# Kernel optimization log

Measured on AMD Instinct MI355X. Metric: run time of the kernel, lower is better.

## Reference

```python
import jax, jax.numpy as jnp
import numpy as np
import math

VOCAB, D, L, B, S = 32000, 1024, 6, 4, 1024
FF = 4 * D


def sinusoidal_pe(max_len, d_model):
    pos = np.arange(max_len)[:, None].astype(np.float32)
    div = np.exp(np.arange(0, d_model, 2).astype(np.float32) * (-math.log(10000.0) / d_model))
    pe = np.zeros((max_len, d_model), dtype=np.float32)
    pe[:, 0::2] = np.sin(pos * div)
    pe[:, 1::2] = np.cos(pos * div)
    return jnp.asarray(pe)


def layernorm(x, g, b, eps=1e-5):
    mu = jnp.mean(x, axis=-1, keepdims=True)
    var = jnp.mean(jnp.square(x - mu), axis=-1, keepdims=True)
    return (x - mu) * jax.lax.rsqrt(var + eps) * g + b


def setup_inputs() -> dict:
    key = jax.random.key(0)
    ks = jax.random.split(key, 16)
    s = 0.02
    inp = {
        "input_ids": jax.random.randint(ks[0], (B, S), 0, VOCAB, dtype=jnp.int32),
        "attention_mask": jnp.ones((B, S), dtype=jnp.int32),
        "emb": jax.random.normal(ks[1], (VOCAB, D), jnp.float32) * s,
        "Wq": jax.random.normal(ks[2], (L, D, D), jnp.float32) * s,
        "Wk": jax.random.normal(ks[3], (L, D, D), jnp.float32) * s,
        "Wv": jax.random.normal(ks[4], (L, D, D), jnp.float32) * s,
        "bq": jnp.zeros((L, D), jnp.float32),
        "bk": jnp.zeros((L, D), jnp.float32),
        "bv": jnp.zeros((L, D), jnp.float32),
        "g1": jnp.ones((L, D), jnp.float32),
        "beta1": jnp.zeros((L, D), jnp.float32),
        "Wf1": jax.random.normal(ks[5], (L, D, FF), jnp.float32) * s,
        "bf1": jnp.zeros((L, FF), jnp.float32),
        "Wf2": jax.random.normal(ks[6], (L, FF, D), jnp.float32) * s,
        "bf2": jnp.zeros((L, D), jnp.float32),
        "g2": jnp.ones((L, D), jnp.float32),
        "beta2": jnp.zeros((L, D), jnp.float32),
    }
    return inp


def reference(input_ids, attention_mask, emb, Wq, Wk, Wv, bq, bk, bv,
              g1, beta1, Wf1, bf1, Wf2, bf2, g2, beta2):
    pe = sinusoidal_pe(1024, D)
    x = emb[input_ids] + pe[: input_ids.shape[1]]           # [B,S,D]
    mask = (attention_mask[:, None, :] != 0)                # [B,1,S]
    scale = 1.0 / math.sqrt(D)
    for l in range(L):
        Q = jnp.einsum('bsd,de->bse', x, Wq[l]) + bq[l]
        K = jnp.einsum('bsd,de->bse', x, Wk[l]) + bk[l]
        V = jnp.einsum('bsd,de->bse', x, Wv[l]) + bv[l]
        scores = jnp.einsum('bqd,bkd->bqk', Q, K) * scale   # [B,S,S]
        scores = jnp.where(mask, scores, -1e9)
        attn = jax.nn.softmax(scores, axis=-1)
        a = jnp.einsum('bqk,bkd->bqd', attn, V)
        x = layernorm(x + a, g1[l], beta1[l])
        h = jax.nn.relu(jnp.einsum('bsd,df->bsf', x, Wf1[l]) + bf1[l])
        f = jnp.einsum('bsf,fd->bsd', h, Wf2[l]) + bf2[l]
        x = layernorm(x + f, g2[l], beta2[l])
    return x
```

## Files before the change

kernel.cpp:

```cpp
#include <hip/hip_runtime.h>

typedef __bf16 bf16_t;
typedef __bf16 bf16x8 __attribute__((ext_vector_type(8)));
typedef float f32x4 __attribute__((ext_vector_type(4)));
typedef unsigned short u16;

#define DEV static __device__ __forceinline__

DEV float bf2f(u16 u) { __bf16 h = __builtin_bit_cast(__bf16, u); return (float)h; }
DEV u16 f2bf(float f) { __bf16 h = (__bf16)f; return __builtin_bit_cast(u16, h); }

DEV void gll16(bf16_t* lds, const bf16_t* g) {
    __builtin_amdgcn_global_load_lds(
        (const __attribute__((address_space(1))) void*)g,
        (__attribute__((address_space(3))) void*)lds, 16, 0, 0);
}

#define WAITV(N) asm volatile("s_waitcnt vmcnt(" #N ")" ::: "memory")

template <int EPI>
__global__ __launch_bounds__(512, 1)
void gemm8p(const bf16_t* __restrict__ A, int lda,
            const bf16_t* __restrict__ Bt, int ldb,
            bf16_t* __restrict__ C, int ldc,
            const float* __restrict__ bias, int K,
            long kadv, long cadv)
{
    __shared__ bf16_t Asm[2 * 2 * 8192];
    __shared__ bf16_t Bsm[2 * 2 * 8192];
    const int tid = threadIdx.x, w = tid >> 6, l = tid & 63;
    const int z = blockIdx.z;
    A  += (size_t)z * kadv;
    Bt += (size_t)z * kadv;
    C  += (size_t)z * cadv;

    const int gx = gridDim.x;
    int lin = blockIdx.y * gx + blockIdx.x;
    const int nlin = gx * gridDim.y;
    lin = (lin & 7) * (nlin >> 3) + (lin >> 3);
    const size_t row0 = (size_t)(lin / gx) * 256;
    const size_t col0 = (size_t)(lin % gx) * 256;

    const int wr = w >> 2, wc = w & 3;
    const int bh = wc >> 1;
    const int browoff = (wc & 1) * 64;
    const int fr = l & 15, q = l >> 4, sw = l & 7;

    const int srow = w * 8 + (l >> 3);
    const int sslot8 = ((l & 7) ^ ((l >> 3) & 7)) * 8;
    const bf16_t* AgH0 = A  + (row0 + srow) * (size_t)lda + sslot8;
    const bf16_t* BgH0 = Bt + (col0 + srow) * (size_t)ldb + sslot8;
    const size_t a128 = (size_t)128 * lda, b128 = (size_t)128 * ldb;
    const size_t a64  = (size_t)64 * lda,  b64  = (size_t)64 * ldb;
    const int wlds = w * 512;

#define STAGE_PAIR(buf, tt, p)                                                 \
    do {                                                                       \
        const int koff = (tt) * 64;                                            \
        if ((p) == 0) {                                                        \
            gll16(Asm + ((buf)*2+0)*8192 + wlds,        AgH0 + koff);          \
            gll16(Asm + ((buf)*2+0)*8192 + 4096 + wlds, AgH0 + koff + a64);    \
        } else if ((p) == 1) {                                                 \
            gll16(Asm + ((buf)*2+1)*8192 + wlds,        AgH0 + a128 + koff);   \
            gll16(Asm + ((buf)*2+1)*8192 + 4096 + wlds, AgH0 + a128 + koff + a64); \
        } else if ((p) == 2) {                                                 \
            gll16(Bsm + ((buf)*2+0)*8192 + wlds,        BgH0 + koff);          \
            gll16(Bsm + ((buf)*2+0)*8192 + 4096 + wlds, BgH0 + koff + b64);    \
        } else {                                                               \
            gll16(Bsm + ((buf)*2+1)*8192 + wlds,        BgH0 + b128 + koff);   \
            gll16(Bsm + ((buf)*2+1)*8192 + 4096 + wlds, BgH0 + b128 + koff + b64); \
        }                                                                      \
    } while (0)

    f32x4 acc[8][4] = {};
    const int NT = K >> 6;

    STAGE_PAIR(0, 0, 0); STAGE_PAIR(0, 0, 1); STAGE_PAIR(0, 0, 2); STAGE_PAIR(0, 0, 3);
    if (NT > 1) { STAGE_PAIR(1, 1, 0); WAITV(2); } else { WAITV(0); }
    __builtin_amdgcn_sched_barrier(0);
    __builtin_amdgcn_s_barrier();

    bf16x8 aR[4][2], bR[4][2];
    for (int t = 0; t < NT; ++t) {
        const int cur = t & 1, nxt = cur ^ 1;
        const bool hasN1 = (t + 1 < NT), hasN2 = (t + 2 < NT);
        const bf16_t* Ab = Asm + (cur * 2 + wr) * 8192;
        const bf16_t* Bb = Bsm + (cur * 2 + bh) * 8192;

#pragma unroll
        for (int mi = 0; mi < 4; mi++)
#pragma unroll
            for (int kk = 0; kk < 2; kk++)
                aR[mi][kk] = *(const bf16x8*)&Ab[(mi * 16 + fr) * 64 + ((kk * 4 + q) ^ sw) * 8];
#pragma unroll
        for (int ni = 0; ni < 2; ni++)
#pragma unroll
            for (int kk = 0; kk < 2; kk++)
                bR[ni][kk] = *(const bf16x8*)&Bb[(browoff + ni * 16 + fr) * 64 + ((kk * 4 + q) ^ sw) * 8];
        if (hasN1) STAGE_PAIR(nxt, t + 1, 1);
        __builtin_amdgcn_s_barrier();
        __builtin_amdgcn_s_setprio(1);
#pragma unroll
        for (int mi = 0; mi < 4; mi++)
#pragma unroll
            for (int ni = 0; ni < 2; ni++)
#pragma unroll
                for (int kk = 0; kk < 2; kk++)
                    acc[mi][ni] = __builtin_amdgcn_mfma_f32_16x16x32_bf16(aR[mi][kk], bR[ni][kk], acc[mi][ni], 0, 0, 0);
        __builtin_amdgcn_s_setprio(0);
        __builtin_amdgcn_s_barrier();

#pragma unroll
        for (int ni = 2; ni < 4; ni++)
#pragma unroll
            for (int kk = 0; kk < 2; kk++)
                bR[ni][kk] = *(const bf16x8*)&Bb[(browoff + ni * 16 + fr) * 64 + ((kk * 4 + q) ^ sw) * 8];
        if (hasN1) STAGE_PAIR(nxt, t + 1, 2);
        __builtin_amdgcn_s_barrier();
        __builtin_amdgcn_s_setprio(1);
#pragma unroll
        for (int mi = 0; mi < 4; mi++)
#pragma unroll
            for (int ni = 2; ni < 4; ni++)
#pragma unroll
                for (int kk = 0; kk < 2; kk++)
                    acc[mi][ni] = __builtin_amdgcn_mfma_f32_16x16x32_bf16(aR[mi][kk], bR[ni][kk], acc[mi][ni], 0, 0, 0);
        __builtin_amdgcn_s_setprio(0);
        __builtin_amdgcn_s_barrier();

#pragma unroll
        for (int mi = 0; mi < 4; mi++)
#pragma unroll
            for (int kk = 0; kk < 2; kk++)
                aR[mi][kk] = *(const bf16x8*)&Ab[((4 + mi) * 16 + fr) * 64 + ((kk * 4 + q) ^ sw) * 8];
        if (hasN1) STAGE_PAIR(nxt, t + 1, 3);
        __builtin_amdgcn_s_barrier();
        __builtin_amdgcn_s_setprio(1);
#pragma unroll
        for (int mi = 0; mi < 4; mi++)
#pragma unroll
            for (int ni = 0; ni < 2; ni++)
#pragma unroll
                for (int kk = 0; kk < 2; kk++)
                    acc[4 + mi][ni] = __builtin_amdgcn_mfma_f32_16x16x32_bf16(aR[mi][kk], bR[ni][kk], acc[4 + mi][ni], 0, 0, 0);
        __builtin_amdgcn_s_setprio(0);
        __builtin_amdgcn_s_barrier();

        if (hasN2) STAGE_PAIR(cur, t + 2, 0);
        __builtin_amdgcn_s_setprio(1);
#pragma unroll
        for (int mi = 0; mi < 4; mi++)
#pragma unroll
            for (int ni = 2; ni < 4; ni++)
#pragma unroll
                for (int kk = 0; kk < 2; kk++)
                    acc[4 + mi][ni] = __builtin_amdgcn_mfma_f32_16x16x32_bf16(aR[mi][kk], bR[ni][kk], acc[4 + mi][ni], 0, 0, 0);
        __builtin_amdgcn_s_setprio(0);
        if (hasN1) {
            if (hasN2) { WAITV(2); } else { WAITV(0); }
            __builtin_amdgcn_sched_barrier(0);
        }
        __builtin_amdgcn_s_barrier();
    }
#undef STAGE_PAIR

    const int cr = q * 4, cc = fr;
#pragma unroll
    for (int ni = 0; ni < 4; ni++) {
        size_t c = col0 + wc * 64 + ni * 16 + cc;
        float bv = bias ? bias[c] : 0.f;
#pragma unroll
        for (int mi = 0; mi < 8; mi++) {
            size_t r = row0 + wr * 128 + mi * 16 + cr;
#pragma unroll
            for (int j = 0; j < 4; j++) {
                float v = acc[mi][ni][j] + bv;
                if (EPI == 1) v = fmaxf(v, 0.f);
                C[(r + j) * ldc + c] = (bf16_t)v;
            }
        }
    }
}

template <int EPI>
__global__ __launch_bounds__(256)
void gemm_bt(const bf16_t* __restrict__ A, int lda, long sA,
             const bf16_t* __restrict__ Bt, int ldb, long sB,
             void* __restrict__ Cv, int ldc, long sC,
             const float* __restrict__ bias, int K, float scale)
{
    __shared__ bf16_t Alds[128 * 64];
    __shared__ bf16_t Blds[128 * 64];
    const int tid = threadIdx.x, w = tid >> 6, l = tid & 63;
    const int bz = blockIdx.z;

    const int gx = gridDim.x;
    int lin = blockIdx.y * gx + blockIdx.x;
    const int nlin = gx * gridDim.y;
    lin = (lin & 7) * (nlin >> 3) + (lin >> 3);
    const size_t row0 = (size_t)(lin / gx) * 128;
    const size_t col0 = (size_t)(lin % gx) * 128;

    A  += (size_t)bz * sA;
    Bt += (size_t)bz * sB;

    const int lr = l >> 3;
    const int sl = (l & 7) ^ lr;
    const bf16_t* Ag = A  + (row0 + (size_t)(w * 32) + lr) * lda + sl * 8;
    const bf16_t* Bg = Bt + (col0 + (size_t)(w * 32) + lr) * ldb + sl * 8;
    bf16_t* Al = &Alds[(w * 32) * 64];
    bf16_t* Bl = &Blds[(w * 32) * 64];

    const int wm = (w >> 1) * 64, wn = (w & 1) * 64;
    f32x4 acc[4][4] = {};

    for (int k0 = 0; k0 < K; k0 += 64) {
#pragma unroll
        for (int c = 0; c < 4; c++) {
            gll16(Al + c * 8 * 64, Ag + (size_t)(c * 8) * lda + k0);
            gll16(Bl + c * 8 * 64, Bg + (size_t)(c * 8) * ldb + k0);
        }
        __syncthreads();

#pragma unroll
        for (int ks = 0; ks < 2; ks++) {
            bf16x8 afr[4], bfr[4];
#pragma unroll
            for (int i = 0; i < 4; i++) {
                const int fr = i * 16 + (l & 15);
                const int slot = (ks * 4 + (l >> 4)) ^ (l & 7);
                afr[i] = *(const bf16x8*)&Alds[(wm + fr) * 64 + slot * 8];
                bfr[i] = *(const bf16x8*)&Blds[(wn + fr) * 64 + slot * 8];
            }
#pragma unroll
            for (int mi = 0; mi < 4; mi++)
#pragma unroll
                for (int ni = 0; ni < 4; ni++)
                    acc[mi][ni] = __builtin_amdgcn_mfma_f32_16x16x32_bf16(afr[mi], bfr[ni], acc[mi][ni], 0, 0, 0);
        }
        __syncthreads();
    }

    const int cr = (l >> 4) * 4, cc = l & 15;
    if (EPI == 2) {
        float* C = (float*)Cv + (size_t)bz * sC;
#pragma unroll
        for (int mi = 0; mi < 4; mi++)
#pragma unroll
            for (int ni = 0; ni < 4; ni++) {
                size_t r = row0 + wm + mi * 16 + cr;
                size_t c = col0 + wn + ni * 16 + cc;
#pragma unroll
                for (int j = 0; j < 4; j++)
                    C[(r + j) * ldc + c] = acc[mi][ni][j] * scale;
            }
    } else {
        bf16_t* C = (bf16_t*)Cv + (size_t)bz * sC;
#pragma unroll
        for (int ni = 0; ni < 4; ni++) {
            size_t c = col0 + wn + ni * 16 + cc;
            float bv = bias ? bias[c] : 0.f;
#pragma unroll
            for (int mi = 0; mi < 4; mi++) {
                size_t r = row0 + wm + mi * 16 + cr;
#pragma unroll
                for (int j = 0; j < 4; j++) {
                    float v = acc[mi][ni][j] + bv;
                    if (EPI == 1) v = fmaxf(v, 0.f);
                    C[(r + j) * ldc + c] = (bf16_t)v;
                }
            }
        }
    }
}

__global__ __launch_bounds__(256)
void transpose_f32_bf16(const float* __restrict__ in, bf16_t* __restrict__ out,
                        int ldin, int ldout)
{
    __shared__ bf16_t t[64][72];
    const int bx = blockIdx.x * 64;
    const int by = blockIdx.y * 64;
    const int tid = threadIdx.x;
    const int cj = (tid & 15) * 4, ri = tid >> 4;
#pragma unroll
    for (int k = 0; k < 4; k++) {
        int r = ri + k * 16;
        float4 v = *(const float4*)&in[(size_t)(by + r) * ldin + bx + cj];
        ushort4 o = {f2bf(v.x), f2bf(v.y), f2bf(v.z), f2bf(v.w)};
        *(ushort4*)&t[r][cj] = o;
    }
    __syncthreads();
#pragma unroll
    for (int k = 0; k < 4; k++) {
        int i = ri + k * 16;
        ushort4 o;
        o.x = __builtin_bit_cast(u16, t[cj + 0][i]);
        o.y = __builtin_bit_cast(u16, t[cj + 1][i]);
        o.z = __builtin_bit_cast(u16, t[cj + 2][i]);
        o.w = __builtin_bit_cast(u16, t[cj + 3][i]);
        *(ushort4*)&out[(size_t)(bx + i) * ldout + by + cj] = o;
    }
}

__global__ __launch_bounds__(256)
void transpose_bf16(const bf16_t* __restrict__ in, bf16_t* __restrict__ out,
                    int ldin, int ldout, long sin_, long sout_)
{
    __shared__ bf16_t t[64][72];
    in  += (size_t)blockIdx.z * sin_;
    out += (size_t)blockIdx.z * sout_;
    const int bx = blockIdx.x * 64;
    const int by = blockIdx.y * 64;
    const int tid = threadIdx.x;
    const int cj = (tid & 15) * 4, ri = tid >> 4;
#pragma unroll
    for (int k = 0; k < 4; k++) {
        int r = ri + k * 16;
        *(ushort4*)&t[r][cj] = *(const ushort4*)&in[(size_t)(by + r) * ldin + bx + cj];
    }
    __syncthreads();
#pragma unroll
    for (int k = 0; k < 4; k++) {
        int i = ri + k * 16;
        ushort4 o;
        o.x = __builtin_bit_cast(u16, t[cj + 0][i]);
        o.y = __builtin_bit_cast(u16, t[cj + 1][i]);
        o.z = __builtin_bit_cast(u16, t[cj + 2][i]);
        o.w = __builtin_bit_cast(u16, t[cj + 3][i]);
        *(ushort4*)&out[(size_t)(bx + i) * ldout + by + cj] = o;
    }
}

__global__ __launch_bounds__(256)
void embed_kernel(const int* __restrict__ ids, const float* __restrict__ emb,
                  float* __restrict__ x, bf16_t* __restrict__ xb)
{
    const int row = blockIdx.x;
    const int s = row & 1023;
    const int id = ids[row];
    const float* er = emb + (size_t)id * 1024;
    float* xr = x + (size_t)row * 1024;
    bf16_t* br = xb + (size_t)row * 1024;
#pragma unroll
    for (int k = 0; k < 2; k++) {
        int i = threadIdx.x + 256 * k;
        int d = 2 * i;
        float dv = expf((float)d * -0.008994473019508f);
        float ph = (float)s * dv;
        float sv, cv;
        sincosf(ph, &sv, &cv);
        float2 ev = *(const float2*)&er[d];
        float x0 = ev.x + sv;
        float x1 = ev.y + cv;
        float2 xo = {x0, x1};
        *(float2*)&xr[d] = xo;
        ushort2 bo = {f2bf(x0), f2bf(x1)};
        *(ushort2*)&br[d] = bo;
    }
}

__global__ __launch_bounds__(256)
void softmax_kernel(const float* __restrict__ sc, const int* __restrict__ amask,
                    bf16_t* __restrict__ p)
{
    const int row = blockIdx.x * 4 + (threadIdx.x >> 6);
    const int l = threadIdx.x & 63;
    const int b = row >> 10;
    const float* s = sc + (size_t)row * 1024;
    const int* m = amask + (size_t)b * 1024;
    float v[16];
    float mx = -3.0e38f;
#pragma unroll
    for (int i = 0; i < 4; i++) {
        int c = 4 * l + 256 * i;
        float4 sv = *(const float4*)&s[c];
        int4 mv = *(const int4*)&m[c];
        v[4 * i + 0] = mv.x ? sv.x : -1e9f;
        v[4 * i + 1] = mv.y ? sv.y : -1e9f;
        v[4 * i + 2] = mv.z ? sv.z : -1e9f;
        v[4 * i + 3] = mv.w ? sv.w : -1e9f;
        mx = fmaxf(mx, fmaxf(fmaxf(v[4 * i], v[4 * i + 1]), fmaxf(v[4 * i + 2], v[4 * i + 3])));
    }
#pragma unroll
    for (int o = 32; o; o >>= 1) mx = fmaxf(mx, __shfl_xor(mx, o, 64));
    float sum = 0.f;
#pragma unroll
    for (int i = 0; i < 16; i++) { v[i] = __expf(v[i] - mx); sum += v[i]; }
#pragma unroll
    for (int o = 32; o; o >>= 1) sum += __shfl_xor(sum, o, 64);
    float inv = 1.0f / sum;
#pragma unroll
    for (int i = 0; i < 4; i++) {
        int c = 4 * l + 256 * i;
        ushort4 st;
        st.x = f2bf(v[4 * i + 0] * inv);
        st.y = f2bf(v[4 * i + 1] * inv);
        st.z = f2bf(v[4 * i + 2] * inv);
        st.w = f2bf(v[4 * i + 3] * inv);
        *(ushort4*)&p[(size_t)row * 1024 + c] = st;
    }
}

__global__ __launch_bounds__(256)
void ln_kernel(const float* __restrict__ xin, const bf16_t* __restrict__ add,
               const float* __restrict__ g, const float* __restrict__ beta,
               float* __restrict__ xout, bf16_t* __restrict__ bout)
{
    __shared__ float red[8];
    const int row = blockIdx.x;
    const int t = threadIdx.x;
    const size_t base = (size_t)row * 1024 + t * 4;
    float4 xv = *(const float4*)&xin[base];
    ushort4 au = *(const ushort4*)&add[base];
    float tv[4];
    tv[0] = xv.x + bf2f(au.x);
    tv[1] = xv.y + bf2f(au.y);
    tv[2] = xv.z + bf2f(au.z);
    tv[3] = xv.w + bf2f(au.w);
    float s = tv[0] + tv[1] + tv[2] + tv[3];
    float s2 = tv[0] * tv[0] + tv[1] * tv[1] + tv[2] * tv[2] + tv[3] * tv[3];
#pragma unroll
    for (int o = 32; o; o >>= 1) { s += __shfl_xor(s, o, 64); s2 += __shfl_xor(s2, o, 64); }
    if ((t & 63) == 0) { red[t >> 6] = s; red[4 + (t >> 6)] = s2; }
    __syncthreads();
    s = red[0] + red[1] + red[2] + red[3];
    s2 = red[4] + red[5] + red[6] + red[7];
    const float mu = s * (1.f / 1024.f);
    const float var = s2 * (1.f / 1024.f) - mu * mu;
    const float rs = rsqrtf(var + 1e-5f);
    float4 gu = *(const float4*)&g[t * 4];
    float4 bu = *(const float4*)&beta[t * 4];
    float y0 = (tv[0] - mu) * rs * gu.x + bu.x;
    float y1 = (tv[1] - mu) * rs * gu.y + bu.y;
    float y2 = (tv[2] - mu) * rs * gu.z + bu.z;
    float y3 = (tv[3] - mu) * rs * gu.w + bu.w;
    float4 yo = {y0, y1, y2, y3};
    *(float4*)&xout[base] = yo;
    ushort4 ob = {f2bf(y0), f2bf(y1), f2bf(y2), f2bf(y3)};
    *(ushort4*)&bout[base] = ob;
}

__global__ __launch_bounds__(256)
void ln4_kernel(const float* __restrict__ xin, const bf16_t* __restrict__ p,
                long pstride, const float* __restrict__ fbias,
                const float* __restrict__ g, const float* __restrict__ beta,
                float* __restrict__ xout, bf16_t* __restrict__ bout)
{
    __shared__ float red[8];
    const int row = blockIdx.x;
    const int t = threadIdx.x;
    const size_t base = (size_t)row * 1024 + t * 4;
    float4 xv = *(const float4*)&xin[base];
    float4 bb = *(const float4*)&fbias[t * 4];
    float tv[4] = {xv.x + bb.x, xv.y + bb.y, xv.z + bb.z, xv.w + bb.w};
#pragma unroll
    for (int z = 0; z < 4; z++) {
        ushort4 au = *(const ushort4*)&p[(size_t)z * pstride + base];
        tv[0] += bf2f(au.x); tv[1] += bf2f(au.y);
        tv[2] += bf2f(au.z); tv[3] += bf2f(au.w);
    }
    float s = tv[0] + tv[1] + tv[2] + tv[3];
    float s2 = tv[0] * tv[0] + tv[1] * tv[1] + tv[2] * tv[2] + tv[3] * tv[3];
#pragma unroll
    for (int o = 32; o; o >>= 1) { s += __shfl_xor(s, o, 64); s2 += __shfl_xor(s2, o, 64); }
    if ((t & 63) == 0) { red[t >> 6] = s; red[4 + (t >> 6)] = s2; }
    __syncthreads();
    s = red[0] + red[1] + red[2] + red[3];
    s2 = red[4] + red[5] + red[6] + red[7];
    const float mu = s * (1.f / 1024.f);
    const float var = s2 * (1.f / 1024.f) - mu * mu;
    const float rs = rsqrtf(var + 1e-5f);
    float4 gu = *(const float4*)&g[t * 4];
    float4 bu = *(const float4*)&beta[t * 4];
    float y0 = (tv[0] - mu) * rs * gu.x + bu.x;
    float y1 = (tv[1] - mu) * rs * gu.y + bu.y;
    float y2 = (tv[2] - mu) * rs * gu.z + bu.z;
    float y3 = (tv[3] - mu) * rs * gu.w + bu.w;
    float4 yo = {y0, y1, y2, y3};
    *(float4*)&xout[base] = yo;
    ushort4 ob = {f2bf(y0), f2bf(y1), f2bf(y2), f2bf(y3)};
    *(ushort4*)&bout[base] = ob;
}

__global__ __launch_bounds__(256)
void biascat_kernel(const float* __restrict__ bq, const float* __restrict__ bk,
                    const float* __restrict__ bv, float* __restrict__ o)
{
    int i = blockIdx.x * 256 + threadIdx.x;
    o[i] = (i < 1024) ? bq[i] : (i < 2048) ? bk[i - 1024] : bv[i - 2048];
}


extern "C" void kernel_launch(void* const* d_in, const int* in_sizes, int n_in,
                              void* d_out, int out_size, void* d_ws, size_t ws_size,
                              hipStream_t stream)
{
    const int*   ids = (const int*)d_in[0];
    const int*   am  = (const int*)d_in[1];
    const float* emb = (const float*)d_in[2];
    const float* Wq  = (const float*)d_in[3];
    const float* Wk  = (const float*)d_in[4];
    const float* Wv  = (const float*)d_in[5];
    const float* bq  = (const float*)d_in[6];
    const float* bk  = (const float*)d_in[7];
    const float* bv  = (const float*)d_in[8];
    const float* g1  = (const float*)d_in[9];
    const float* be1 = (const float*)d_in[10];
    const float* Wf1 = (const float*)d_in[11];
    const float* bf1 = (const float*)d_in[12];
    const float* Wf2 = (const float*)d_in[13];
    const float* bf2_ = (const float*)d_in[14];
    const float* g2  = (const float*)d_in[15];
    const float* be2 = (const float*)d_in[16];

    char* ws = (char*)d_ws;
    float*  x      = (float*)(ws);
    bf16_t* xb     = (bf16_t*)(ws + (16LL << 20));
    bf16_t* qkv    = (bf16_t*)(ws + (24LL << 20));
    bf16_t* vt     = (bf16_t*)(ws + (48LL << 20));
    bf16_t* fpart  = (bf16_t*)(ws + (24LL << 20));
    float*  scores = (float*)(ws + (56LL << 20));
    bf16_t* p      = (bf16_t*)(ws + (72LL << 20));
    bf16_t* h      = (bf16_t*)(ws + (56LL << 20));
    bf16_t* attn   = (bf16_t*)(ws + (88LL << 20));
    bf16_t* wqkvT  = (bf16_t*)(ws + (96LL << 20));
    bf16_t* wf1T   = (bf16_t*)(ws + (102LL << 20));
    bf16_t* wf2T   = (bf16_t*)(ws + (110LL << 20));
    float*  qbias  = (float*)(ws + (118LL << 20));

    embed_kernel<<<4096, 256, 0, stream>>>(ids, emb, x, xb);

    for (int l = 0; l < 6; l++) {
        const size_t DD = 1024 * 1024;
        transpose_f32_bf16<<<dim3(16, 16, 1), 256, 0, stream>>>(Wq + (size_t)l * DD, wqkvT,          1024, 1024);
        transpose_f32_bf16<<<dim3(16, 16, 1), 256, 0, stream>>>(Wk + (size_t)l * DD, wqkvT + DD,     1024, 1024);
        transpose_f32_bf16<<<dim3(16, 16, 1), 256, 0, stream>>>(Wv + (size_t)l * DD, wqkvT + 2 * DD, 1024, 1024);
        transpose_f32_bf16<<<dim3(64, 16, 1), 256, 0, stream>>>(Wf1 + (size_t)l * 4 * DD, wf1T, 4096, 1024);
        transpose_f32_bf16<<<dim3(16, 64, 1), 256, 0, stream>>>(Wf2 + (size_t)l * 4 * DD, wf2T, 1024, 4096);
        biascat_kernel<<<12, 256, 0, stream>>>(bq + l * 1024, bk + l * 1024, bv + l * 1024, qbias);

        gemm8p<0><<<dim3(12, 16, 1), 512, 0, stream>>>(xb, 1024, wqkvT, 1024,
                                                       qkv, 3072, qbias, 1024, 0, 0);
        transpose_bf16<<<dim3(16, 16, 4), 256, 0, stream>>>(qkv + 2048, vt, 3072, 1024,
                                                            1024L * 3072, 1024L * 1024);
        gemm_bt<2><<<dim3(8, 8, 4), 256, 0, stream>>>(qkv, 3072, 1024L * 3072,
                                                      qkv + 1024, 3072, 1024L * 3072,
                                                      scores, 1024, 1024L * 1024,
                                                      nullptr, 1024, 0.03125f);
        softmax_kernel<<<1024, 256, 0, stream>>>(scores, am, p);
        gemm_bt<0><<<dim3(8, 8, 4), 256, 0, stream>>>(p, 1024, 1024L * 1024,
                                                      vt, 1024, 1024L * 1024,
                                                      attn, 1024, 1024L * 1024,
                                                      nullptr, 1024, 0.f);
        ln_kernel<<<4096, 256, 0, stream>>>(x, attn, g1 + l * 1024, be1 + l * 1024, x, xb);
        gemm8p<1><<<dim3(16, 16, 1), 512, 0, stream>>>(xb, 1024, wf1T, 1024,
                                                       h, 4096, bf1 + l * 4096, 1024, 0, 0);
        gemm8p<0><<<dim3(4, 16, 4), 512, 0, stream>>>(h, 4096, wf2T, 4096,
                                                      fpart, 1024, nullptr, 1024,
                                                      1024, 4096L * 1024);
        float* xo = (l == 5) ? (float*)d_out : x;
        ln4_kernel<<<4096, 256, 0, stream>>>(x, fpart, 4096L * 1024, bf2_ + l * 1024,
                                             g2 + l * 1024, be2 + l * 1024, xo, xb);
    }
    (void)in_sizes; (void)n_in; (void)out_size; (void)ws_size;
}
```

Before: 1.388 ms.

## Double-buffer attention GEMM and batch weight transposes across layers upfront

Replaces the single-buffered attention GEMM with a double-buffered version. It prefetches the next K-tile via global_load_lds while MFMAs run on the current tile, and uses split barriers and s_setprio to favor the math. Separately, all six layers' weight transposes and bias concatenations are hoisted into a few batched launches before the layer loop, which removes about 36 small launches. The cost is double the LDS per block and a much larger workspace footprint for the pre-transposed weights.

```diff
diff --git a/kernel.cpp b/kernel.cpp
--- a/kernel.cpp
+++ b/kernel.cpp
@@ -184,13 +184,13 @@
 
 template <int EPI>
 __global__ __launch_bounds__(256)
-void gemm_bt(const bf16_t* __restrict__ A, int lda, long sA,
+void gemm_db(const bf16_t* __restrict__ A, int lda, long sA,
              const bf16_t* __restrict__ Bt, int ldb, long sB,
              void* __restrict__ Cv, int ldc, long sC,
              const float* __restrict__ bias, int K, float scale)
 {
-    __shared__ bf16_t Alds[128 * 64];
-    __shared__ bf16_t Blds[128 * 64];
+    __shared__ bf16_t Asm[2][128 * 64];
+    __shared__ bf16_t Bsm[2][128 * 64];
     const int tid = threadIdx.x, w = tid >> 6, l = tid & 63;
     const int bz = blockIdx.z;
 
@@ -208,40 +208,79 @@
     const int sl = (l & 7) ^ lr;
     const bf16_t* Ag = A  + (row0 + (size_t)(w * 32) + lr) * lda + sl * 8;
     const bf16_t* Bg = Bt + (col0 + (size_t)(w * 32) + lr) * ldb + sl * 8;
-    bf16_t* Al = &Alds[(w * 32) * 64];
-    bf16_t* Bl = &Blds[(w * 32) * 64];
+    const int wlds = (w * 32) * 64;
+
+#define STA(buf, tt)                                                           \
+    do { const int ko = (tt) * 64;                                             \
+        _Pragma("unroll")                                                      \
+        for (int c = 0; c < 4; c++)                                            \
+            gll16(&Asm[buf][wlds + c * 8 * 64], Ag + (size_t)(c * 8) * lda + ko); \
+    } while (0)
+#define STB(buf, tt)                                                           \
+    do { const int ko = (tt) * 64;                                             \
+        _Pragma("unroll")                                                      \
+        for (int c = 0; c < 4; c++)                                            \
+            gll16(&Bsm[buf][wlds + c * 8 * 64], Bg + (size_t)(c * 8) * ldb + ko); \
+    } while (0)
 
     const int wm = (w >> 1) * 64, wn = (w & 1) * 64;
+    const int fr16 = l & 15, q4 = l >> 4, sw = l & 7;
     f32x4 acc[4][4] = {};
-
-    for (int k0 = 0; k0 < K; k0 += 64) {
-#pragma unroll
-        for (int c = 0; c < 4; c++) {
-            gll16(Al + c * 8 * 64, Ag + (size_t)(c * 8) * lda + k0);
-            gll16(Bl + c * 8 * 64, Bg + (size_t)(c * 8) * ldb + k0);
+    const int NT = K >> 6;
+
+    STA(0, 0); STB(0, 0);
+    if (NT > 1) { STA(1, 1); WAITV(4); } else { WAITV(0); }
+    __builtin_amdgcn_sched_barrier(0);
+    __builtin_amdgcn_s_barrier();
+
+    for (int t = 0; t < NT; ++t) {
+        const int cur = t & 1, nxt = cur ^ 1;
+        const bool hasN1 = (t + 1 < NT), hasN2 = (t + 2 < NT);
+
+        bf16x8 a0[4], b0[4];
+#pragma unroll
+        for (int i = 0; i < 4; i++) {
+            const int slot = (q4 ^ sw) * 8;
+            a0[i] = *(const bf16x8*)&Asm[cur][(wm + i * 16 + fr16) * 64 + slot];
+            b0[i] = *(const bf16x8*)&Bsm[cur][(wn + i * 16 + fr16) * 64 + slot];
         }
-        __syncthreads();
-
-#pragma unroll
-        for (int ks = 0; ks < 2; ks++) {
-            bf16x8 afr[4], bfr[4];
-#pragma unroll
-            for (int i = 0; i < 4; i++) {
-                const int fr = i * 16 + (l & 15);
-                const int slot = (ks * 4 + (l >> 4)) ^ (l & 7);
-                afr[i] = *(const bf16x8*)&Alds[(wm + fr) * 64 + slot * 8];
-                bfr[i] = *(const bf16x8*)&Blds[(wn + fr) * 64 + slot * 8];
-            }
-#pragma unroll
-            for (int mi = 0; mi < 4; mi++)
-#pragma unroll
-                for (int ni = 0; ni < 4; ni++)
-                    acc[mi][ni] = __builtin_amdgcn_mfma_f32_16x16x32_bf16(afr[mi], bfr[ni], acc[mi][ni], 0, 0, 0);
+        if (hasN1) STB(nxt, t + 1);
+        __builtin_amdgcn_s_barrier();
+        __builtin_amdgcn_s_setprio(1);
+#pragma unroll
+        for (int mi = 0; mi < 4; mi++)
+#pragma unroll
+            for (int ni = 0; ni < 4; ni++)
+                acc[mi][ni] = __builtin_amdgcn_mfma_f32_16x16x32_bf16(a0[mi], b0[ni], acc[mi][ni], 0, 0, 0);
+        __builtin_amdgcn_s_setprio(0);
+        __builtin_amdgcn_s_barrier();
+
+        bf16x8 a1[4], b1[4];
+#pragma unroll
+        for (int i = 0; i < 4; i++) {
+            const int slot = ((4 + q4) ^ sw) * 8;
+            a1[i] = *(const bf16x8*)&Asm[cur][(wm + i * 16 + fr16) * 64 + slot];
+            b1[i] = *(const bf16x8*)&Bsm[cur][(wn + i * 16 + fr16) * 64 + slot];
         }
-        __syncthreads();
-    }
-
-    const int cr = (l >> 4) * 4, cc = l & 15;
+        __builtin_amdgcn_s_barrier();
+        __builtin_amdgcn_s_setprio(1);
+#pragma unroll
+        for (int mi = 0; mi < 4; mi++)
+#pragma unroll
+            for (int ni = 0; ni < 4; ni++)
+                acc[mi][ni] = __builtin_amdgcn_mfma_f32_16x16x32_bf16(a1[mi], b1[ni], acc[mi][ni], 0, 0, 0);
+        __builtin_amdgcn_s_setprio(0);
+        if (hasN2) STA(cur, t + 2);
+        if (hasN1) {
+            if (hasN2) { WAITV(4); } else { WAITV(0); }
+            __builtin_amdgcn_sched_barrier(0);
+        }
+        __builtin_amdgcn_s_barrier();
+    }
+#undef STA
+#undef STB
+
+    const int cr = q4 * 4, cc = fr16;
     if (EPI == 2) {
         float* C = (float*)Cv + (size_t)bz * sC;
 #pragma unroll
@@ -276,9 +315,11 @@
 
 __global__ __launch_bounds__(256)
 void transpose_f32_bf16(const float* __restrict__ in, bf16_t* __restrict__ out,
-                        int ldin, int ldout)
+                        int ldin, int ldout, long sin_, long sout_)
 {
     __shared__ bf16_t t[64][72];
+    in  += (size_t)blockIdx.z * sin_;
+    out += (size_t)blockIdx.z * sout_;
     const int bx = blockIdx.x * 64;
     const int by = blockIdx.y * 64;
     const int tid = threadIdx.x;
@@ -484,11 +525,14 @@
 }
 
 __global__ __launch_bounds__(256)
-void biascat_kernel(const float* __restrict__ bq, const float* __restrict__ bk,
-                    const float* __restrict__ bv, float* __restrict__ o)
+void biascat6_kernel(const float* __restrict__ bq, const float* __restrict__ bk,
+                     const float* __restrict__ bv, float* __restrict__ o)
 {
     int i = blockIdx.x * 256 + threadIdx.x;
-    o[i] = (i < 1024) ? bq[i] : (i < 2048) ? bk[i - 1024] : bv[i - 2048];
+    int lyr = i / 3072, j = i - lyr * 3072;
+    o[i] = (j < 1024) ? bq[lyr * 1024 + j]
+         : (j < 2048) ? bk[lyr * 1024 + j - 1024]
+                      : bv[lyr * 1024 + j - 2048];
 }
 
 
@@ -524,39 +568,40 @@
     bf16_t* p      = (bf16_t*)(ws + (72LL << 20));
     bf16_t* h      = (bf16_t*)(ws + (56LL << 20));
     bf16_t* attn   = (bf16_t*)(ws + (88LL << 20));
-    bf16_t* wqkvT  = (bf16_t*)(ws + (96LL << 20));
-    bf16_t* wf1T   = (bf16_t*)(ws + (102LL << 20));
-    bf16_t* wf2T   = (bf16_t*)(ws + (110LL << 20));
-    float*  qbias  = (float*)(ws + (118LL << 20));
+    bf16_t* wqkvTA = (bf16_t*)(ws + (96LL << 20));
+    bf16_t* wf1TA  = (bf16_t*)(ws + (132LL << 20));
+    bf16_t* wf2TA  = (bf16_t*)(ws + (180LL << 20));
+    float*  qbiasA = (float*)(ws + (228LL << 20));
+
+    const size_t DD = 1024 * 1024;
+
+    transpose_f32_bf16<<<dim3(16, 16, 6), 256, 0, stream>>>(Wq, wqkvTA,          1024, 1024, (long)DD, 3L * DD);
+    transpose_f32_bf16<<<dim3(16, 16, 6), 256, 0, stream>>>(Wk, wqkvTA + DD,     1024, 1024, (long)DD, 3L * DD);
+    transpose_f32_bf16<<<dim3(16, 16, 6), 256, 0, stream>>>(Wv, wqkvTA + 2 * DD, 1024, 1024, (long)DD, 3L * DD);
+    transpose_f32_bf16<<<dim3(64, 16, 6), 256, 0, stream>>>(Wf1, wf1TA, 4096, 1024, 4L * DD, 4L * DD);
+    transpose_f32_bf16<<<dim3(16, 64, 6), 256, 0, stream>>>(Wf2, wf2TA, 1024, 4096, 4L * DD, 4L * DD);
+    biascat6_kernel<<<72, 256, 0, stream>>>(bq, bk, bv, qbiasA);
 
     embed_kernel<<<4096, 256, 0, stream>>>(ids, emb, x, xb);
 
     for (int l = 0; l < 6; l++) {
-        const size_t DD = 1024 * 1024;
-        transpose_f32_bf16<<<dim3(16, 16, 1), 256, 0, stream>>>(Wq + (size_t)l * DD, wqkvT,          1024, 1024);
-        transpose_f32_bf16<<<dim3(16, 16, 1), 256, 0, stream>>>(Wk + (size_t)l * DD, wqkvT + DD,     1024, 1024);
-        transpose_f32_bf16<<<dim3(16, 16, 1), 256, 0, stream>>>(Wv + (size_t)l * DD, wqkvT + 2 * DD, 1024, 1024);
-        transpose_f32_bf16<<<dim3(64, 16, 1), 256, 0, stream>>>(Wf1 + (size_t)l * 4 * DD, wf1T, 4096, 1024);
-        transpose_f32_bf16<<<dim3(16, 64, 1), 256, 0, stream>>>(Wf2 + (size_t)l * 4 * DD, wf2T, 1024, 4096);
-        biascat_kernel<<<12, 256, 0, stream>>>(bq + l * 1024, bk + l * 1024, bv + l * 1024, qbias);
-
-        gemm8p<0><<<dim3(12, 16, 1), 512, 0, stream>>>(xb, 1024, wqkvT, 1024,
-                                                       qkv, 3072, qbias, 1024, 0, 0);
+        gemm8p<0><<<dim3(12, 16, 1), 512, 0, stream>>>(xb, 1024, wqkvTA + (size_t)l * 3 * DD, 1024,
+                                                       qkv, 3072, qbiasA + l * 3072, 1024, 0, 0);
         transpose_bf16<<<dim3(16, 16, 4), 256, 0, stream>>>(qkv + 2048, vt, 3072, 1024,
                                                             1024L * 3072, 1024L * 1024);
-        gemm_bt<2><<<dim3(8, 8, 4), 256, 0, stream>>>(qkv, 3072, 1024L * 3072,
+        gemm_db<2><<<dim3(8, 8, 4), 256, 0, stream>>>(qkv, 3072, 1024L * 3072,
                                                       qkv + 1024, 3072, 1024L * 3072,
                                                       scores, 1024, 1024L * 1024,
                                                       nullptr, 1024, 0.03125f);
         softmax_kernel<<<1024, 256, 0, stream>>>(scores, am, p);
-        gemm_bt<0><<<dim3(8, 8, 4), 256, 0, stream>>>(p, 1024, 1024L * 1024,
+        gemm_db<0><<<dim3(8, 8, 4), 256, 0, stream>>>(p, 1024, 1024L * 1024,
                                                       vt, 1024, 1024L * 1024,
                                                       attn, 1024, 1024L * 1024,
                                                       nullptr, 1024, 0.f);
         ln_kernel<<<4096, 256, 0, stream>>>(x, attn, g1 + l * 1024, be1 + l * 1024, x, xb);
-        gemm8p<1><<<dim3(16, 16, 1), 512, 0, stream>>>(xb, 1024, wf1T, 1024,
+        gemm8p<1><<<dim3(16, 16, 1), 512, 0, stream>>>(xb, 1024, wf1TA + (size_t)l * 4 * DD, 1024,
                                                        h, 4096, bf1 + l * 4096, 1024, 0, 0);
-        gemm8p<0><<<dim3(4, 16, 4), 512, 0, stream>>>(h, 4096, wf2T, 4096,
+        gemm8p<0><<<dim3(4, 16, 4), 512, 0, stream>>>(h, 4096, wf2TA + (size_t)l * 4 * DD, 4096,
                                                       fpart, 1024, nullptr, 1024,
                                                       1024, 4096L * 1024);
         float* xo = (l == 5) ? (float*)d_out : x;
```

Measured after the change: 1.352 ms. -2.6%, faster.
